# Optimization experiments

Measured on AMD Instinct MI355X. Metric: run time of the kernel, lower is better.

## Reference

```python
import jax, jax.numpy as jnp
import numpy as np

PARTITIONS = [1, 2, 4, 8, 16, 32]
FORECAST = 720
D_MODEL = 256
B, C = 64, 64


def len_of_split_into_k_parts(L, k):
    avg, rem = L // k, L % k
    return [avg + (1 if i < rem else 0) for i in range(k)]


def setup_inputs() -> dict:
    key = jax.random.key(0)
    keys = jax.random.split(key, 1 + 2 * len(PARTITIONS))
    T = sum(PARTITIONS)
    inp = {"x": jax.random.normal(keys[0], (B, C, T, D_MODEL), dtype=jnp.float32)}
    for i, k in enumerate(PARTITIONS):
        max_len = max(len_of_split_into_k_parts(FORECAST, k))
        bound = 1.0 / np.sqrt(D_MODEL)
        inp[f"W{i}"] = jax.random.uniform(keys[1 + 2 * i], (max_len, D_MODEL), minval=-bound, maxval=bound, dtype=jnp.float32)
        inp[f"b{i}"] = jax.random.uniform(keys[2 + 2 * i], (max_len,), minval=-bound, maxval=bound, dtype=jnp.float32)
    return inp


def _forward(x, Ws, bs):
    idx = 0
    total = None
    for i, k in enumerate(PARTITIONS):
        split = len_of_split_into_k_parts(FORECAST, k)
        x_r = x[..., idx:idx + k, :]                      # [B, C, k, d]
        idx += k
        proj = jnp.einsum('bctd,md->bctm', x_r, Ws[i]) + bs[i]  # [B, C, k, max_len]
        # ragged slice+concat: token s contributes its first split[s] positions
        tok = np.repeat(np.arange(k), split)              # [f] static indices
        pos = np.concatenate([np.arange(s) for s in split])  # [f]
        res = proj[..., tok, pos]                         # [B, C, f]
        total = res if total is None else total + res
    return jnp.swapaxes(total, -1, -2)                    # [B, f, C]


def reference(x, W0, b0, W1, b1, W2, b2, W3, b3, W4, b4, W5, b5):
    Ws = [W0, W1, W2, W3, W4, W5]
    bs = [b0, b1, b2, b3, b4, b5]
    return _forward(x, Ws, bs)
```

## Files before the change

### kernel.cpp

```cpp
#include <hip/hip_runtime.h>
#include <stdint.h>


#define FDIM 720
#define DDIM 256
#define TDIM 63
#define NSUBTOT 299
#define TAB_BYTES ((size_t)NSUBTOT * 8 * 1024)
#define OUTELEMS ((size_t)64 * FDIM * 64)
#define NPREPTHR (NSUBTOT * 8 * 64)

typedef __attribute__((ext_vector_type(8))) short short8;
typedef __attribute__((ext_vector_type(4))) float f32x4;

__device__ __forceinline__ uint32_t pkru(float a, float b) {
    uint32_t ua = __builtin_bit_cast(uint32_t, a) + 0x8000u;
    uint32_t ub = __builtin_bit_cast(uint32_t, b) + 0x8000u;
    return __builtin_amdgcn_perm(ub, ua, 0x07060302u);
}
__device__ __forceinline__ short8 loadpack(const float* p) {
    float4 v0 = *(const float4*)p;
    float4 v1 = *(const float4*)(p + 4);
    uint4 u;
    u.x = pkru(v0.x, v0.y);
    u.y = pkru(v0.z, v0.w);
    u.z = pkru(v1.x, v1.y);
    u.w = pkru(v1.z, v1.w);
    return __builtin_bit_cast(short8, u);
}

__device__ __forceinline__ void atomAddF(float* p, float v) {
    unsafeAtomicAdd(p, v);
}

__device__ __forceinline__ void jpos(int i, int f, int& j, int& pos) {
    switch (i) {
        case 0: j = 0;       pos = f;            break;
        case 1: j = f / 360; pos = f - 360 * j;  break;
        case 2: j = f / 180; pos = f - 180 * j;  break;
        case 3: j = f / 90;  pos = f - 90 * j;   break;
        case 4: j = f / 45;  pos = f - 45 * j;   break;
        default:
            if (f < 368) { j = f / 23;  pos = f - 23 * j; }
            else { int g = f - 368; int q = g / 22; j = 16 + q; pos = g - 22 * q; }
            break;
    }
}

__device__ __forceinline__ void tok_params(int tok, int& len, int& ns,
                                           int& start, int& tabsub) {
    if (tok < 1)       { len = 720; ns = 45; start = 0;
                         tabsub = 0; }
    else if (tok < 3)  { int j = tok - 1;  len = 360; ns = 23; start = 360 * j;
                         tabsub = 45 + j * 23; }
    else if (tok < 7)  { int j = tok - 3;  len = 180; ns = 12; start = 180 * j;
                         tabsub = 91 + j * 12; }
    else if (tok < 15) { int j = tok - 7;  len = 90;  ns = 6;  start = 90 * j;
                         tabsub = 139 + j * 6; }
    else if (tok < 31) { int j = tok - 15; len = 45;  ns = 3;  start = 45 * j;
                         tabsub = 187 + j * 3; }
    else               { int j = tok - 31;
                         len = (j < 16) ? 23 : 22;
                         start = (j < 16) ? 23 * j : 368 + 22 * (j - 16);
                         ns = 2; tabsub = 235 + j * 2; }
}

__global__ __launch_bounds__(256) void olrs_prepinit(
    const float* __restrict__ W0, const float* __restrict__ W1,
    const float* __restrict__ W2, const float* __restrict__ W3,
    const float* __restrict__ W4, const float* __restrict__ W5,
    const float* __restrict__ b0, const float* __restrict__ b1,
    const float* __restrict__ b2, const float* __restrict__ b3,
    const float* __restrict__ b4, const float* __restrict__ b5,
    char* __restrict__ ws, float* __restrict__ out)
{
    const int gid = blockIdx.x * 256 + threadIdx.x;

    const size_t base = (size_t)gid * 4;
    if (base < OUTELEMS) {
        const int f = (int)((base >> 6) % FDIM);
        int j, p;
        float s = b0[f];
        jpos(1, f, j, p); s += b1[p];
        jpos(2, f, j, p); s += b2[p];
        jpos(3, f, j, p); s += b3[p];
        jpos(4, f, j, p); s += b4[p];
        jpos(5, f, j, p); s += b5[p];
        float4 o = {s, s, s, s};
        *(float4*)(out + base) = o;
    }

    if (gid < NPREPTHR) {
        const int lane = gid & 63;
        const int fid  = gid >> 6;
        const int ks = fid & 7;
        const int g  = fid >> 3;

        int len; const float* W; int s;
        if (g < 45)       { W = W0; len = 720; s = g; }
        else if (g < 91)  { int g2 = g - 45;  W = W1; len = 360; s = g2 % 23; }
        else if (g < 139) { int g2 = g - 91;  W = W2; len = 180; s = g2 % 12; }
        else if (g < 187) { int g2 = g - 139; W = W3; len = 90;  s = g2 % 6; }
        else if (g < 235) { int g2 = g - 187; W = W4; len = 45;  s = g2 % 3; }
        else              { int g2 = g - 235; W = W5; int j = g2 >> 1;
                            len = (j < 16) ? 23 : 22; s = g2 & 1; }

        const int m15  = lane & 15;
        const int koct = lane >> 4;
        const int pos  = s * 16 + m15;
        uint4 u = {0u, 0u, 0u, 0u};
        if (pos < len) {
            const float* src = W + (size_t)pos * DDIM + ks * 32 + koct * 8;
            float4 v0 = *(const float4*)src;
            float4 v1 = *(const float4*)(src + 4);
            u.x = pkru(v0.x, v0.y);
            u.y = pkru(v0.z, v0.w);
            u.z = pkru(v1.x, v1.y);
            u.w = pkru(v1.z, v1.w);
        }
        *(uint4*)(ws + (size_t)fid * 1024 + lane * 16) = u;
    }
}

__global__ __launch_bounds__(256) void olrs_main8(
    const float* __restrict__ x,
    const char* __restrict__ ws,
    float* __restrict__ out)
{
    __shared__ char lds[32768];

    const int bid   = blockIdx.x;
    const int rid   = bid >> 7;
    const int ntile = bid & 127;
    const int w     = threadIdx.x >> 6;
    const int lane  = threadIdx.x & 63;
    const int b     = ntile >> 1;
    const int c0    = (ntile & 1) << 5;
    const int m15   = lane & 15;
    const int koct  = lane >> 4;

    int tok, s0, slab;
    bool shx;
    if (rid < 2)      { tok = 0;            s0 = rid * 24 + w * 6; shx = true;  slab = 0; }
    else if (rid < 4) { tok = rid - 1;      s0 = w * 6;            shx = true;  slab = 0; }
    else if (rid < 6) { int tb = 3 + (rid - 4) * 2;
                        tok = tb + (w >> 1); s0 = (w & 1) * 6;     shx = true;  slab = w >> 1; }
    else              { tok = 7 + (rid - 6) * 4 + w; s0 = 0;       shx = false; slab = 0; }

    int len, ns, start, tabsub;
    tok_params(tok, len, ns, start, tabsub);
    const int send = (s0 + 6 < ns) ? (s0 + 6) : ns;

    short8 xl[8], xh[8];
    if (shx) {
        const int nslab   = (rid >= 4 && rid < 6) ? 2 : 1;
        const int tokbase = (rid < 2) ? 0 : ((rid < 4) ? (rid - 1) : 3 + (rid - 4) * 2);
        const int cc = threadIdx.x >> 3;
        const int t8 = threadIdx.x & 7;
        for (int sl = 0; sl < nslab; sl++) {
            const float* src = x + (((size_t)(b * 64 + c0 + cc)) * TDIM + tokbase + sl) * DDIM;
            char* dst = lds + sl * 16384;
            #pragma unroll
            for (int rep = 0; rep < 4; rep++) {
                const int d8 = t8 + rep * 8;
                float4 v0 = *(const float4*)(src + d8 * 8);
                float4 v1 = *(const float4*)(src + d8 * 8 + 4);
                uint4 u;
                u.x = pkru(v0.x, v0.y);
                u.y = pkru(v0.z, v0.w);
                u.z = pkru(v1.x, v1.y);
                u.w = pkru(v1.z, v1.w);
                const int slot = ((d8 >> 2) * 2 + (cc >> 4)) * 64
                               + (d8 & 3) * 16 + (cc & 15);
                *(uint4*)(dst + slot * 16) = u;
            }
        }
        __syncthreads();
        const char* sb = lds + slab * 16384;
        #pragma unroll
        for (int ks = 0; ks < 8; ks++) {
            xl[ks] = *(const short8*)(sb + ((ks * 2 + 0) * 64 + lane) * 16);
            xh[ks] = *(const short8*)(sb + ((ks * 2 + 1) * 64 + lane) * 16);
        }
    } else {
        const float* xpl = x + (((size_t)(b * 64 + c0 + m15)) * TDIM + tok) * DDIM;
        const float* xph = xpl + (size_t)16 * TDIM * DDIM;
        #pragma unroll
        for (int ks = 0; ks < 8; ks++)
            xl[ks] = loadpack(xpl + ks * 32 + koct * 8);
        #pragma unroll
        for (int ks = 0; ks < 8; ks++)
            xh[ks] = loadpack(xph + ks * 32 + koct * 8);
    }

    const char* tab = ws + (size_t)tabsub * 8192 + lane * 16;
    float* obl = out + ((size_t)b * FDIM + start) * 64 + c0 + m15;
    float* obh = obl + 16;

    short8 wA[8], wB[8];

    auto loadW = [&](short8* wreg, int s) {
        const char* t = tab + (size_t)s * 8192;
        #pragma unroll
        for (int ks = 0; ks < 8; ks++)
            wreg[ks] = *(const short8*)(t + ks * 1024);
    };
    auto compute = [&](const short8* wreg, int s) {
        f32x4 al0 = {0.f, 0.f, 0.f, 0.f}, al1 = {0.f, 0.f, 0.f, 0.f};
        f32x4 ah0 = {0.f, 0.f, 0.f, 0.f}, ah1 = {0.f, 0.f, 0.f, 0.f};
        #pragma unroll
        for (int ks = 0; ks < 8; ks += 2) {
            al0 = __builtin_amdgcn_mfma_f32_16x16x32_bf16(wreg[ks],     xl[ks],     al0, 0, 0, 0);
            ah0 = __builtin_amdgcn_mfma_f32_16x16x32_bf16(wreg[ks],     xh[ks],     ah0, 0, 0, 0);
            al1 = __builtin_amdgcn_mfma_f32_16x16x32_bf16(wreg[ks + 1], xl[ks + 1], al1, 0, 0, 0);
            ah1 = __builtin_amdgcn_mfma_f32_16x16x32_bf16(wreg[ks + 1], xh[ks + 1], ah1, 0, 0, 0);
        }
        const int fl0 = s * 16 + koct * 4;
        #pragma unroll
        for (int rg = 0; rg < 4; rg++) {
            const int fl = fl0 + rg;
            if (fl < len) {
                atomAddF(obl + (size_t)fl * 64, al0[rg] + al1[rg]);
                atomAddF(obh + (size_t)fl * 64, ah0[rg] + ah1[rg]);
            }
        }
    };

    int s = s0;
    loadW(wA, s);
    for (;;) {
        if (s + 1 < send) loadW(wB, s + 1);
        compute(wA, s);
        if (++s >= send) break;
        if (s + 1 < send) loadW(wA, s + 1);
        compute(wB, s);
        if (++s >= send) break;
    }
}

__device__ __forceinline__ int startf(int i, int j) {
    switch (i) {
        case 0: return 0;
        case 1: return 360 * j;
        case 2: return 180 * j;
        case 3: return 90 * j;
        case 4: return 45 * j;
        default: return (j < 16) ? 23 * j : 368 + 22 * (j - 16);
    }
}

__global__ __launch_bounds__(256) void olrs_fb(
    const float* __restrict__ x,
    const float* __restrict__ W0, const float* __restrict__ b0,
    const float* __restrict__ W1, const float* __restrict__ b1,
    const float* __restrict__ W2, const float* __restrict__ b2,
    const float* __restrict__ W3, const float* __restrict__ b3,
    const float* __restrict__ W4, const float* __restrict__ b4,
    const float* __restrict__ W5, const float* __restrict__ b5,
    float* __restrict__ out)
{
    const float* Wp[6] = {W0, W1, W2, W3, W4, W5};
    const float* bp[6] = {b0, b1, b2, b3, b4, b5};
    const int TB[6] = {0, 1, 3, 7, 15, 31};

    const int wid  = blockIdx.x * 4 + (threadIdx.x >> 6);
    const int lane = threadIdx.x & 63;
    const int ft   = wid % 45;
    const int bc   = wid / 45;
    const int b    = bc >> 2;
    const int c0   = (bc & 3) << 4;
    const int f0   = ft << 4;
    const int m15  = lane & 15;
    const int koct = lane >> 4;
    const size_t xrow = (size_t)(b * 64 + c0 + m15) * TDIM;

    f32x4 acc = {0.f, 0.f, 0.f, 0.f};
    #pragma unroll
    for (int i = 0; i < 6; i++) {
        int jlo, plo, jhi, phi;
        jpos(i, f0, jlo, plo);
        jpos(i, f0 + 15, jhi, phi);
        const bool cross = (jhi > jlo);
        const int fb = cross ? (startf(i, jhi) - f0) : 16;
        const float* xlo = x + (xrow + TB[i] + jlo) * DDIM;
        const float* xhi = x + (xrow + TB[i] + jhi) * DDIM;
        int jw, pw;
        jpos(i, f0 + m15, jw, pw);
        const float* wsrc = Wp[i] + (size_t)pw * DDIM;
        #pragma unroll
        for (int ks = 0; ks < 8; ks++) {
            const int d0 = ks * 32 + koct * 8;
            short8 a = loadpack(wsrc + d0);
            short8 blo = loadpack(xlo + d0);
            if (!cross) {
                acc = __builtin_amdgcn_mfma_f32_16x16x32_bf16(a, blo, acc, 0, 0, 0);
            } else {
                short8 bhi = loadpack(xhi + d0);
                short8 z;
                #pragma unroll
                for (int q = 0; q < 8; q++) z[q] = 0;
                short8 alo = (m15 < fb) ? a : z;
                short8 ahi = (m15 < fb) ? z : a;
                acc = __builtin_amdgcn_mfma_f32_16x16x32_bf16(alo, blo, acc, 0, 0, 0);
                acc = __builtin_amdgcn_mfma_f32_16x16x32_bf16(ahi, bhi, acc, 0, 0, 0);
            }
        }
    }
    #pragma unroll
    for (int rg = 0; rg < 4; rg++) {
        const int f = f0 + koct * 4 + rg;
        float bias = 0.f;
        #pragma unroll
        for (int i = 0; i < 6; i++) {
            int j, pos;
            jpos(i, f, j, pos);
            bias += bp[i][pos];
        }
        out[((size_t)b * FDIM + f) * 64 + c0 + m15] = acc[rg] + bias;
    }
}

extern "C" void kernel_launch(void* const* d_in, const int* in_sizes, int n_in,
                              void* d_out, int out_size, void* d_ws, size_t ws_size,
                              hipStream_t stream) {
    (void)in_sizes; (void)n_in; (void)out_size;

    const float* x  = (const float*)d_in[0];
    const float* W0 = (const float*)d_in[1];
    const float* b0 = (const float*)d_in[2];
    const float* W1 = (const float*)d_in[3];
    const float* b1 = (const float*)d_in[4];
    const float* W2 = (const float*)d_in[5];
    const float* b2 = (const float*)d_in[6];
    const float* W3 = (const float*)d_in[7];
    const float* b3 = (const float*)d_in[8];
    const float* W4 = (const float*)d_in[9];
    const float* b4 = (const float*)d_in[10];
    const float* W5 = (const float*)d_in[11];
    const float* b5 = (const float*)d_in[12];
    float* out = (float*)d_out;

    if (ws_size >= TAB_BYTES) {
        char* ws = (char*)d_ws;
        olrs_prepinit<<<dim3((unsigned)(OUTELEMS / 4 / 256)), dim3(256), 0, stream>>>(
            W0, W1, W2, W3, W4, W5, b0, b1, b2, b3, b4, b5, ws, out);
        olrs_main8<<<dim3(20 * 128), dim3(256), 0, stream>>>(x, ws, out);
    } else {
        olrs_fb<<<dim3(45 * 256), dim3(256), 0, stream>>>(
            x, W0, b0, W1, b1, W2, b2, W3, b3, W4, b4, W5, b5, out);
    }
}
```

Measured before the change: 86.93 us.

## Fold k=32 partition into prep kernel with direct stores replacing bias-init pass

```diff
diff --git a/kernel.cpp b/kernel.cpp
--- a/kernel.cpp
+++ b/kernel.cpp
@@ -5,10 +5,10 @@
 #define FDIM 720
 #define DDIM 256
 #define TDIM 63
-#define NSUBTOT 299
-#define TAB_BYTES ((size_t)NSUBTOT * 8 * 1024)
+#define NSUB5 235
+#define TAB_BYTES ((size_t)NSUB5 * 8 * 1024)
 #define OUTELEMS ((size_t)64 * FDIM * 64)
-#define NPREPTHR (NSUBTOT * 8 * 64)
+#define NPREPBLK 470
 
 typedef __attribute__((ext_vector_type(8))) short short8;
 typedef __attribute__((ext_vector_type(4))) float f32x4;
@@ -57,15 +57,28 @@
                          tabsub = 91 + j * 12; }
     else if (tok < 15) { int j = tok - 7;  len = 90;  ns = 6;  start = 90 * j;
                          tabsub = 139 + j * 6; }
-    else if (tok < 31) { int j = tok - 15; len = 45;  ns = 3;  start = 45 * j;
+    else               { int j = tok - 15; len = 45;  ns = 3;  start = 45 * j;
                          tabsub = 187 + j * 3; }
-    else               { int j = tok - 31;
-                         len = (j < 16) ? 23 : 22;
-                         start = (j < 16) ? 23 * j : 368 + 22 * (j - 16);
-                         ns = 2; tabsub = 235 + j * 2; }
-}
-
-__global__ __launch_bounds__(256) void olrs_prepinit(
+}
+
+__device__ __forceinline__ float bias_sum(
+    int f,
+    const float* __restrict__ b0, const float* __restrict__ b1,
+    const float* __restrict__ b2, const float* __restrict__ b3,
+    const float* __restrict__ b4, const float* __restrict__ b5)
+{
+    int j, p;
+    float s = b0[f];
+    jpos(1, f, j, p); s += b1[p];
+    jpos(2, f, j, p); s += b2[p];
+    jpos(3, f, j, p); s += b3[p];
+    jpos(4, f, j, p); s += b4[p];
+    jpos(5, f, j, p); s += b5[p];
+    return s;
+}
+
+__global__ __launch_bounds__(256) void olrs_k32(
+    const float* __restrict__ x,
     const float* __restrict__ W0, const float* __restrict__ W1,
     const float* __restrict__ W2, const float* __restrict__ W3,
     const float* __restrict__ W4, const float* __restrict__ W5,
@@ -74,23 +87,10 @@
     const float* __restrict__ b4, const float* __restrict__ b5,
     char* __restrict__ ws, float* __restrict__ out)
 {
-    const int gid = blockIdx.x * 256 + threadIdx.x;
-
-    const size_t base = (size_t)gid * 4;
-    if (base < OUTELEMS) {
-        const int f = (int)((base >> 6) % FDIM);
-        int j, p;
-        float s = b0[f];
-        jpos(1, f, j, p); s += b1[p];
-        jpos(2, f, j, p); s += b2[p];
-        jpos(3, f, j, p); s += b3[p];
-        jpos(4, f, j, p); s += b4[p];
-        jpos(5, f, j, p); s += b5[p];
-        float4 o = {s, s, s, s};
-        *(float4*)(out + base) = o;
-    }
-
-    if (gid < NPREPTHR) {
+    const int bid = blockIdx.x;
+
+    if (bid < NPREPBLK) {
+        const int gid  = bid * 256 + threadIdx.x;
         const int lane = gid & 63;
         const int fid  = gid >> 6;
         const int ks = fid & 7;
@@ -101,16 +101,14 @@
         else if (g < 91)  { int g2 = g - 45;  W = W1; len = 360; s = g2 % 23; }
         else if (g < 139) { int g2 = g - 91;  W = W2; len = 180; s = g2 % 12; }
         else if (g < 187) { int g2 = g - 139; W = W3; len = 90;  s = g2 % 6; }
-        else if (g < 235) { int g2 = g - 187; W = W4; len = 45;  s = g2 % 3; }
-        else              { int g2 = g - 235; W = W5; int j = g2 >> 1;
-                            len = (j < 16) ? 23 : 22; s = g2 & 1; }
-
-        const int m15  = lane & 15;
-        const int koct = lane >> 4;
-        const int pos  = s * 16 + m15;
+        else              { int g2 = g - 187; W = W4; len = 45;  s = g2 % 3; }
+
+        const int m15p  = lane & 15;
+        const int koctp = lane >> 4;
+        const int pos   = s * 16 + m15p;
         uint4 u = {0u, 0u, 0u, 0u};
         if (pos < len) {
-            const float* src = W + (size_t)pos * DDIM + ks * 32 + koct * 8;
+            const float* src = W + (size_t)pos * DDIM + ks * 32 + koctp * 8;
             float4 v0 = *(const float4*)src;
             float4 v1 = *(const float4*)(src + 4);
             u.x = pkru(v0.x, v0.y);
@@ -120,9 +118,81 @@
         }
         *(uint4*)(ws + (size_t)fid * 1024 + lane * 16) = u;
     }
-}
-
-__global__ __launch_bounds__(256) void olrs_main8(
+
+    const int wid   = bid * 4 + (threadIdx.x >> 6);
+    const int lane  = threadIdx.x & 63;
+    const int tq    = wid >> 7;
+    const int ntile = wid & 127;
+    const int tok   = 31 + tq;
+    const int b     = ntile >> 1;
+    const int c0    = (ntile & 1) << 5;
+    const int m15   = lane & 15;
+    const int koct  = lane >> 4;
+
+    const int len   = (tq < 16) ? 23 : 22;
+    const int start = (tq < 16) ? 23 * tq : 368 + 22 * (tq - 16);
+
+    const float* xpl = x + (((size_t)(b * 64 + c0 + m15)) * TDIM + tok) * DDIM;
+    const float* xph = xpl + (size_t)16 * TDIM * DDIM;
+    short8 xl[8], xh[8];
+    #pragma unroll
+    for (int ks = 0; ks < 8; ks++)
+        xl[ks] = loadpack(xpl + ks * 32 + koct * 8);
+    #pragma unroll
+    for (int ks = 0; ks < 8; ks++)
+        xh[ks] = loadpack(xph + ks * 32 + koct * 8);
+
+    float* obl = out + ((size_t)b * FDIM + start) * 64 + c0 + m15;
+    float* obh = obl + 16;
+
+    short8 wA[8], wB[8];
+
+    auto loadWr = [&](short8* wreg, int s) {
+        const int pos = s * 16 + m15;
+        if (pos < len) {
+            const float* p = W5 + (size_t)pos * DDIM + koct * 8;
+            #pragma unroll
+            for (int ks = 0; ks < 8; ks++)
+                wreg[ks] = loadpack(p + ks * 32);
+        } else {
+            #pragma unroll
+            for (int ks = 0; ks < 8; ks++) {
+                short8 z;
+                #pragma unroll
+                for (int q = 0; q < 8; q++) z[q] = 0;
+                wreg[ks] = z;
+            }
+        }
+    };
+    auto computeStore = [&](const short8* wreg, int s) {
+        f32x4 al0 = {0.f, 0.f, 0.f, 0.f}, al1 = {0.f, 0.f, 0.f, 0.f};
+        f32x4 ah0 = {0.f, 0.f, 0.f, 0.f}, ah1 = {0.f, 0.f, 0.f, 0.f};
+        #pragma unroll
+        for (int ks = 0; ks < 8; ks += 2) {
+            al0 = __builtin_amdgcn_mfma_f32_16x16x32_bf16(wreg[ks],     xl[ks],     al0, 0, 0, 0);
+            ah0 = __builtin_amdgcn_mfma_f32_16x16x32_bf16(wreg[ks],     xh[ks],     ah0, 0, 0, 0);
+            al1 = __builtin_amdgcn_mfma_f32_16x16x32_bf16(wreg[ks + 1], xl[ks + 1], al1, 0, 0, 0);
+            ah1 = __builtin_amdgcn_mfma_f32_16x16x32_bf16(wreg[ks + 1], xh[ks + 1], ah1, 0, 0, 0);
+        }
+        const int fl0 = s * 16 + koct * 4;
+        #pragma unroll
+        for (int rg = 0; rg < 4; rg++) {
+            const int fl = fl0 + rg;
+            if (fl < len) {
+                const float bias = bias_sum(start + fl, b0, b1, b2, b3, b4, b5);
+                obl[(size_t)fl * 64] = al0[rg] + al1[rg] + bias;
+                obh[(size_t)fl * 64] = ah0[rg] + ah1[rg] + bias;
+            }
+        }
+    };
+
+    loadWr(wA, 0);
+    loadWr(wB, 1);
+    computeStore(wA, 0);
+    computeStore(wB, 1);
+}
+
+__global__ __launch_bounds__(256) void olrs_mainB(
     const float* __restrict__ x,
     const char* __restrict__ ws,
     float* __restrict__ out)
@@ -141,11 +211,12 @@
 
     int tok, s0, slab;
     bool shx;
-    if (rid < 2)      { tok = 0;            s0 = rid * 24 + w * 6; shx = true;  slab = 0; }
-    else if (rid < 4) { tok = rid - 1;      s0 = w * 6;            shx = true;  slab = 0; }
+    if (rid < 2)      { tok = 0;             s0 = rid * 24 + w * 6; shx = true;  slab = 0; }
+    else if (rid < 4) { tok = rid - 1;       s0 = w * 6;            shx = true;  slab = 0; }
     else if (rid < 6) { int tb = 3 + (rid - 4) * 2;
-                        tok = tb + (w >> 1); s0 = (w & 1) * 6;     shx = true;  slab = w >> 1; }
-    else              { tok = 7 + (rid - 6) * 4 + w; s0 = 0;       shx = false; slab = 0; }
+                        tok = tb + (w >> 1); s0 = (w & 1) * 6;      shx = true;  slab = w >> 1; }
+    else if (rid < 8) { tok = 7 + (rid - 6) * 4 + w;  s0 = 0;       shx = false; slab = 0; }
+    else              { tok = 15 + (rid - 8) * 4 + w; s0 = 0;       shx = false; slab = 0; }
 
     int len, ns, start, tabsub;
     tok_params(tok, len, ns, start, tabsub);
@@ -153,7 +224,7 @@
 
     short8 xl[8], xh[8];
     if (shx) {
-        const int nslab   = (rid >= 4 && rid < 6) ? 2 : 1;
+        const int nslab   = (rid >= 4) ? 2 : 1;
         const int tokbase = (rid < 2) ? 0 : ((rid < 4) ? (rid - 1) : 3 + (rid - 4) * 2);
         const int cc = threadIdx.x >> 3;
         const int t8 = threadIdx.x & 7;
@@ -238,6 +309,7 @@
     }
 }
 
+__device__ __forceinline__ void jpos6(int i, int f, int& j, int& pos) { jpos(i, f, j, pos); }
 __device__ __forceinline__ int startf(int i, int j) {
     switch (i) {
         case 0: return 0;
@@ -278,14 +350,14 @@
     #pragma unroll
     for (int i = 0; i < 6; i++) {
         int jlo, plo, jhi, phi;
-        jpos(i, f0, jlo, plo);
-        jpos(i, f0 + 15, jhi, phi);
+        jpos6(i, f0, jlo, plo);
+        jpos6(i, f0 + 15, jhi, phi);
         const bool cross = (jhi > jlo);
         const int fb = cross ? (startf(i, jhi) - f0) : 16;
         const float* xlo = x + (xrow + TB[i] + jlo) * DDIM;
         const float* xhi = x + (xrow + TB[i] + jhi) * DDIM;
         int jw, pw;
-        jpos(i, f0 + m15, jw, pw);
+        jpos6(i, f0 + m15, jw, pw);
         const float* wsrc = Wp[i] + (size_t)pw * DDIM;
         #pragma unroll
         for (int ks = 0; ks < 8; ks++) {
@@ -313,7 +385,7 @@
         #pragma unroll
         for (int i = 0; i < 6; i++) {
             int j, pos;
-            jpos(i, f, j, pos);
+            jpos6(i, f, j, pos);
             bias += bp[i][pos];
         }
         out[((size_t)b * FDIM + f) * 64 + c0 + m15] = acc[rg] + bias;
@@ -342,9 +414,9 @@
 
     if (ws_size >= TAB_BYTES) {
         char* ws = (char*)d_ws;
-        olrs_prepinit<<<dim3((unsigned)(OUTELEMS / 4 / 256)), dim3(256), 0, stream>>>(
-            W0, W1, W2, W3, W4, W5, b0, b1, b2, b3, b4, b5, ws, out);
-        olrs_main8<<<dim3(20 * 128), dim3(256), 0, stream>>>(x, ws, out);
+        olrs_k32<<<dim3(1024), dim3(256), 0, stream>>>(
+            x, W0, W1, W2, W3, W4, W5, b0, b1, b2, b3, b4, b5, ws, out);
+        olrs_mainB<<<dim3(12 * 128), dim3(256), 0, stream>>>(x, ws, out);
     } else {
         olrs_fb<<<dim3(45 * 256), dim3(256), 0, stream>>>(
             x, W0, b0, W1, b1, W2, b2, W3, b3, W4, b4, W5, b5, out);
```

Result: slower. 95.98 us (+10.4%).
